# Optimization experiments

Hardware: AMD Instinct MI355X
Metric: run time of the kernel (lower is better)

The kernel has to match this reference:

```python
import jax, jax.numpy as jnp
import numpy as np

N_HEADS = 32
N_KV_HEADS = 8
HEAD_DIM = 128
GROUP = N_HEADS // N_KV_HEADS  # 4
MAX_SEQ_LEN = 4096
DIM = 3072
NEG_BIG = 1.0e9


def setup_inputs() -> dict:
    key = jax.random.key(0)
    ks = jax.random.split(key, 8)
    B, T = 1, 2048
    return {
        "x": jax.random.normal(ks[0], (B, T, DIM), dtype=jnp.float32),
        "freqs_cos": jax.random.uniform(ks[1], (T, HEAD_DIM // 2), dtype=jnp.float32),
        "freqs_sin": jax.random.uniform(ks[2], (T, HEAD_DIM // 2), dtype=jnp.float32),
        "input_pos": jnp.arange(T, dtype=jnp.int32),
        "wq": jax.random.normal(ks[3], (N_HEADS * HEAD_DIM, DIM), dtype=jnp.float32) * 0.02,
        "wk": jax.random.normal(ks[4], (N_KV_HEADS * HEAD_DIM, DIM), dtype=jnp.float32) * 0.02,
        "wv": jax.random.normal(ks[5], (N_KV_HEADS * HEAD_DIM, DIM), dtype=jnp.float32) * 0.02,
        "wo": jax.random.normal(ks[6], (DIM, N_HEADS * HEAD_DIM), dtype=jnp.float32) * 0.02,
        "k_cache": jnp.zeros((1, N_KV_HEADS, MAX_SEQ_LEN, HEAD_DIM), dtype=jnp.float32),
        "v_cache": jnp.zeros((1, N_KV_HEADS, MAX_SEQ_LEN, HEAD_DIM), dtype=jnp.float32),
    }


def _rotate_half(x):
    half = x.shape[-1] // 2
    return jnp.concatenate([-x[..., half:], x[..., :half]], axis=-1)


def _apply_rope(q, k, freqs_cos, freqs_sin):
    # freqs: [T, D/2] -> [1, T, 1, D] (tiled x2, matching torch repeat on last dim)
    fc = jnp.concatenate([freqs_cos, freqs_cos], axis=-1)[None, :, None, :]
    fs = jnp.concatenate([freqs_sin, freqs_sin], axis=-1)[None, :, None, :]
    qf = q.astype(jnp.float32)
    kf = k.astype(jnp.float32)
    q_out = qf * fc + _rotate_half(qf) * fs
    k_out = kf * fc + _rotate_half(kf) * fs
    return q_out.astype(q.dtype), k_out.astype(k.dtype)


def reference(x, freqs_cos, freqs_sin, input_pos, wq, wk, wv, wo, k_cache, v_cache):
    B, T, _ = x.shape
    # QKV projections
    q = (x @ wq.T).reshape(B, T, N_HEADS, HEAD_DIM)
    k = (x @ wk.T).reshape(B, T, N_KV_HEADS, HEAD_DIM)
    v = (x @ wv.T).reshape(B, T, N_KV_HEADS, HEAD_DIM)
    # split-half RoPE (computed in fp32)
    q, k = _apply_rope(q, k, freqs_cos, freqs_sin)
    # StaticKVCache.update: scatter [B,H,T,D] into [1,H,S,D] cache at input_pos (dim 2)
    kc = k_cache.at[:, :, input_pos].set(k.transpose(0, 2, 1, 3))
    vc = v_cache.at[:, :, input_pos].set(v.transpose(0, 2, 1, 3))
    # MetalSDPA: additive causal mask over full cache length
    S = kc.shape[2]
    k_pos = jnp.arange(S)
    valid = jnp.clip(input_pos[:, None] - k_pos[None, :] + 1, 0, 1)  # [T, S]
    mask = (valid.astype(q.dtype) - 1.0) * NEG_BIG
    # GQA attention: group q heads per kv head
    qg = q.transpose(0, 2, 1, 3).reshape(B, N_KV_HEADS, GROUP, T, HEAD_DIM)
    scale = 1.0 / jnp.sqrt(jnp.asarray(HEAD_DIM, dtype=q.dtype))
    scores = jnp.einsum('bhgtd,bhsd->bhgts', qg, kc) * scale + mask  # [B,Hk,G,T,S]
    attn = jax.nn.softmax(scores, axis=-1)
    y = jnp.einsum('bhgts,bhsd->bhgtd', attn, vc)
    y = y.reshape(B, N_HEADS, T, HEAD_DIM).transpose(0, 2, 1, 3).reshape(B, T, N_HEADS * HEAD_DIM)
    return y @ wo.T
```

## Files before the change

### kernel.cpp

```cpp
#include <hip/hip_runtime.h>

typedef __attribute__((ext_vector_type(8))) short bf16x8;
typedef __attribute__((ext_vector_type(4))) float f32x4;

#define T_SEQ   2048
#define DIM     3072
#define NQH     32
#define NKVH    8
#define HD      128
#define QDIM    4096
#define KVDIM   1024

#define AS1 __attribute__((address_space(1)))
#define AS3 __attribute__((address_space(3)))

static __device__ __forceinline__ unsigned short f2bf(float f) {
  unsigned u = __float_as_uint(f);
  u += 0x7FFFu + ((u >> 16) & 1u);
  return (unsigned short)(u >> 16);
}
static __device__ __forceinline__ float bf2f(unsigned short h) {
  return __uint_as_float(((unsigned)h) << 16);
}
static __device__ __forceinline__ unsigned pkbf(float lo, float hi) {
  unsigned r;
  asm("v_cvt_pk_bf16_f32 %0, %1, %2" : "=v"(r) : "v"(lo), "v"(hi));
  return r;
}

static __device__ __forceinline__ void gload_lds16(const unsigned short* g, unsigned short* l) {
  __builtin_amdgcn_global_load_lds((AS1 void*)(g), (AS3 void*)(l), 16, 0, 0);
}

__global__ void cvt_all(const float* __restrict__ x,  const float* __restrict__ wq,
                        const float* __restrict__ wk, const float* __restrict__ wv,
                        unsigned short* __restrict__ xb,
                        unsigned short* __restrict__ wqkvb) {
  const int N0 = 1572864;
  const int E1 = N0 + 3145728;
  const int E2 = E1 + 786432;
  const int E3 = E2 + 786432;
  const int stride = gridDim.x * blockDim.x;
  for (int i = blockIdx.x * blockDim.x + threadIdx.x; i < E3; i += stride) {
    const float* s; unsigned short* d; int off;
    if (i < N0)      { s = x;  d = xb;               off = i; }
    else if (i < E1) { s = wq; d = wqkvb;            off = i - N0; }
    else if (i < E2) { s = wk; d = wqkvb + 12582912; off = i - E1; }
    else             { s = wv; d = wqkvb + 15728640; off = i - E2; }
    float4 v = reinterpret_cast<const float4*>(s)[off];
    ushort4 o;
    o.x = f2bf(v.x); o.y = f2bf(v.y); o.z = f2bf(v.z); o.w = f2bf(v.w);
    reinterpret_cast<ushort4*>(d + (size_t)off * 4)[0] = o;
  }
}

__global__ __launch_bounds__(256) void gemm_qkv(
    const unsigned short* __restrict__ A, const unsigned short* __restrict__ B,
    const float* __restrict__ fc, const float* __restrict__ fs,
    unsigned short* __restrict__ qo, unsigned short* __restrict__ ko,
    unsigned short* __restrict__ vt,
    const float* __restrict__ wo, unsigned short* __restrict__ wob) {
  if (blockIdx.x >= 768) {
    const int total = 3145728;
    for (int i = (blockIdx.x - 768) * 256 + threadIdx.x; i < total; i += 32768) {
      float4 v = reinterpret_cast<const float4*>(wo)[i];
      ushort4 o;
      o.x = f2bf(v.x); o.y = f2bf(v.y); o.z = f2bf(v.z); o.w = f2bf(v.w);
      reinterpret_cast<ushort4*>(wob + (size_t)i * 4)[0] = o;
    }
    return;
  }
  __shared__ unsigned short epi[128 * 132];
  unsigned short* la = epi;
  unsigned short* lb = epi + 8192;
  const int K = DIM, nbx = 48;
  int bid = blockIdx.x;
  bid = (bid & 7) * 96 + (bid >> 3);
  const int bx = bid % nbx, by = bid / nbx;
  const int tid = threadIdx.x;
  const int ln = tid & 63;
  const int wave = tid >> 6;
  const int lr = ln & 15, lg = ln >> 4;
  const int rowA0 = by << 7, rowB0 = bx << 7;

  f32x4 acc[2][8] = {};

  const int ktn = K >> 6;
  for (int kt = 0; kt < ktn; kt++) {
    __syncthreads();
#pragma unroll
    for (int it = 0; it < 4; it++) {
      int ci = it * 256 + tid;
      int r = ci >> 3, cpos = ci & 7;
      int c = cpos ^ (r & 7);
      gload_lds16(A + (size_t)(rowA0 + r) * K + kt * 64 + c * 8, &la[ci * 8]);
      gload_lds16(B + (size_t)(rowB0 + r) * K + kt * 64 + c * 8, &lb[ci * 8]);
    }
    __syncthreads();
#pragma unroll
    for (int kk = 0; kk < 2; kk++) {
      bf16x8 af_[2], bf_[8];
#pragma unroll
      for (int mi = 0; mi < 2; mi++) {
        int r = wave * 32 + mi * 16 + lr;
        int p = (kk * 4 + lg) ^ (r & 7);
        af_[mi] = *reinterpret_cast<const bf16x8*>(&la[r * 64 + p * 8]);
      }
#pragma unroll
      for (int ni = 0; ni < 8; ni++) {
        int r = ni * 16 + lr;
        int p = (kk * 4 + lg) ^ (r & 7);
        bf_[ni] = *reinterpret_cast<const bf16x8*>(&lb[r * 64 + p * 8]);
      }
#pragma unroll
      for (int mi = 0; mi < 2; mi++)
#pragma unroll
        for (int ni = 0; ni < 8; ni++)
          acc[mi][ni] = __builtin_amdgcn_mfma_f32_16x16x32_bf16(af_[mi], bf_[ni], acc[mi][ni], 0, 0, 0);
    }
  }

  if (bx < 40) {
    unsigned short* dst; int dstride;
    if (bx < 32) { dst = qo + (size_t)bx * 128; dstride = QDIM; }
    else         { dst = ko + (size_t)(bx - 32) * 128; dstride = KVDIM; }
#pragma unroll
    for (int mi = 0; mi < 2; mi++)
#pragma unroll
      for (int j = 0; j < 4; j++) {
        int t = rowA0 + wave * 32 + mi * 16 + lg * 4 + j;
#pragma unroll
        for (int ni = 0; ni < 4; ni++) {
          int d = ni * 16 + lr;
          float c = fc[t * 64 + d], s = fs[t * 64 + d];
          float x0 = acc[mi][ni][j], x1 = acc[mi][ni + 4][j];
          dst[(size_t)t * dstride + d]      = f2bf(x0 * c - x1 * s);
          dst[(size_t)t * dstride + d + 64] = f2bf(x1 * c + x0 * s);
        }
      }
  } else {
    __syncthreads();
#pragma unroll
    for (int mi = 0; mi < 2; mi++)
#pragma unroll
      for (int ni = 0; ni < 8; ni++)
#pragma unroll
        for (int j = 0; j < 4; j++) {
          int r = wave * 32 + mi * 16 + lg * 4 + j;
          int cc = ni * 16 + lr;
          epi[r * 132 + cc] = f2bf(acc[mi][ni][j]);
        }
    __syncthreads();
    const int ccol = tid >> 1, th = tid & 1;
    size_t vrow = (size_t)((bx - 40) * 128 + ccol) * T_SEQ + rowA0 + th * 64;
#pragma unroll
    for (int i = 0; i < 16; i++) {
      ushort4 o;
      o.x = epi[(th * 64 + i * 4 + 0) * 132 + ccol];
      o.y = epi[(th * 64 + i * 4 + 1) * 132 + ccol];
      o.z = epi[(th * 64 + i * 4 + 2) * 132 + ccol];
      o.w = epi[(th * 64 + i * 4 + 3) * 132 + ccol];
      *reinterpret_cast<ushort4*>(&vt[vrow + i * 4]) = o;
    }
  }
}

__global__ __launch_bounds__(256) void gemm_bt(
    const unsigned short* __restrict__ A, const unsigned short* __restrict__ B,
    float* __restrict__ Cf, int M, int N, int K) {
  __shared__ unsigned short la[128 * 64];
  __shared__ unsigned short lb[128 * 64];
  const int nbx = N >> 7;
  const int q8 = gridDim.x >> 3;
  int bid = blockIdx.x;
  bid = (bid & 7) * q8 + (bid >> 3);
  const int bx = bid % nbx, by = bid / nbx;
  const int tid = threadIdx.x;
  const int ln = tid & 63;
  const int wave = tid >> 6;
  const int lr = ln & 15, lg = ln >> 4;
  const int wr = wave >> 1, wc = wave & 1;
  const int rowA0 = by << 7, rowB0 = bx << 7;

  f32x4 acc[4][4] = {};

  const int ktn = K >> 6;
  for (int kt = 0; kt < ktn; kt++) {
    __syncthreads();
#pragma unroll
    for (int it = 0; it < 4; it++) {
      int ci = it * 256 + tid;
      int r = ci >> 3, cpos = ci & 7;
      int c = cpos ^ (r & 7);
      gload_lds16(A + (size_t)(rowA0 + r) * K + kt * 64 + c * 8, &la[ci * 8]);
      gload_lds16(B + (size_t)(rowB0 + r) * K + kt * 64 + c * 8, &lb[ci * 8]);
    }
    __syncthreads();
#pragma unroll
    for (int kk = 0; kk < 2; kk++) {
      bf16x8 af[4], bfr[4];
#pragma unroll
      for (int mi = 0; mi < 4; mi++) {
        int r = wr * 64 + mi * 16 + lr;
        int p = (kk * 4 + lg) ^ (r & 7);
        af[mi] = *reinterpret_cast<const bf16x8*>(&la[r * 64 + p * 8]);
      }
#pragma unroll
      for (int ni = 0; ni < 4; ni++) {
        int r = wc * 64 + ni * 16 + lr;
        int p = (kk * 4 + lg) ^ (r & 7);
        bfr[ni] = *reinterpret_cast<const bf16x8*>(&lb[r * 64 + p * 8]);
      }
#pragma unroll
      for (int mi = 0; mi < 4; mi++)
#pragma unroll
        for (int ni = 0; ni < 4; ni++)
          acc[mi][ni] = __builtin_amdgcn_mfma_f32_16x16x32_bf16(af[mi], bfr[ni], acc[mi][ni], 0, 0, 0);
    }
  }
#pragma unroll
  for (int mi = 0; mi < 4; mi++)
#pragma unroll
    for (int ni = 0; ni < 4; ni++)
#pragma unroll
      for (int j = 0; j < 4; j++) {
        int r = rowA0 + wr * 64 + mi * 16 + lg * 4 + j;
        int cc = rowB0 + wc * 64 + ni * 16 + lr;
        Cf[(size_t)r * N + cc] = acc[mi][ni][j];
      }
}

__global__ __launch_bounds__(256) void attn_fwd(
    const unsigned short* __restrict__ q, const unsigned short* __restrict__ k,
    const unsigned short* __restrict__ vt, unsigned short* __restrict__ y) {
  __shared__ unsigned short k_lds[2][32 * 128];
  __shared__ unsigned short v_lds[2][128 * 32];
  __shared__ unsigned short p_lds[4][16 * 40];
  __shared__ float a_lds[4][16];
  const int tid = threadIdx.x;
  const int ln = tid & 63;
  const int wave = tid >> 6;
  const int lr = ln & 15, lg = ln >> 4;

  const int kh = blockIdx.x & 7;
  const int i = blockIdx.x >> 3;
  const int qh = i & 3;
  const int pr = i >> 2;
  const int qta = pr, qtb = 31 - pr;
  const int h = kh * 4 + qh;

  const int qra0 = qta * 64 + wave * 16, qrowa = qra0 + lr;
  const int qrb0 = qtb * 64 + wave * 16, qrowb = qrb0 + lr;
  const float SL2E = 0.08838834764831845f * 1.44269504088896f;
  const float NEGINF = -__builtin_inff();

  bf16x8 qfa[4], qfb[4];
  {
    const unsigned short* qba = q + (size_t)qrowa * QDIM + h * HD + lg * 8;
    const unsigned short* qbb = q + (size_t)qrowb * QDIM + h * HD + lg * 8;
#pragma unroll
    for (int dc = 0; dc < 4; dc++) {
      qfa[dc] = *reinterpret_cast<const bf16x8*>(qba + dc * 32);
      qfb[dc] = *reinterpret_cast<const bf16x8*>(qbb + dc * 32);
    }
  }

  f32x4 acca[8] = {}, accb[8] = {};
  float ma = NEGINF, la = 0.f, mb = NEGINF, lb = 0.f;

  const int krow0 = tid >> 4,  kcol0 = tid & 15;
  const int krow1 = 16 + krow0;
  const int vrow0 = tid >> 2,  vcol0 = tid & 3;
  const int vrow1 = 64 + vrow0;

  auto tile_compute = [&](int sb, int cur, const bf16x8 (&qf)[4], f32x4 (&acc)[8],
                          float& m, float& lsum, int qr0, int qrow) {
    f32x4 s0t = {0.f, 0.f, 0.f, 0.f}, s1t = {0.f, 0.f, 0.f, 0.f};
    __builtin_amdgcn_s_setprio(1);
#pragma unroll
    for (int dc = 0; dc < 4; dc++) {
      int c = lg + dc * 4;
      int p = c ^ (lr & 7);
      bf16x8 a0 = *reinterpret_cast<const bf16x8*>(&k_lds[cur][lr * 128 + p * 8]);
      bf16x8 a1 = *reinterpret_cast<const bf16x8*>(&k_lds[cur][(lr + 16) * 128 + p * 8]);
      s0t = __builtin_amdgcn_mfma_f32_16x16x32_bf16(a0, qf[dc], s0t, 0, 0, 0);
      s1t = __builtin_amdgcn_mfma_f32_16x16x32_bf16(a1, qf[dc], s1t, 0, 0, 0);
    }
    __builtin_amdgcn_s_setprio(0);

    float vv[8];
    if (sb + 31 <= qr0) {
#pragma unroll
      for (int jj = 0; jj < 4; jj++) { vv[jj] = s0t[jj]; vv[jj + 4] = s1t[jj]; }
    } else {
      const int base0 = sb + lg * 4;
#pragma unroll
      for (int jj = 0; jj < 4; jj++) {
        vv[jj]     = (base0 + jj      <= qrow) ? s0t[jj] : NEGINF;
        vv[jj + 4] = (base0 + jj + 16 <= qrow) ? s1t[jj] : NEGINF;
      }
    }

    float mx = fmaxf(fmaxf(fmaxf(vv[0], vv[1]), fmaxf(vv[2], vv[3])),
                     fmaxf(fmaxf(vv[4], vv[5]), fmaxf(vv[6], vv[7])));
    mx = fmaxf(mx, __shfl_xor(mx, 16));
    mx = fmaxf(mx, __shfl_xor(mx, 32));

    const bool doresc = __any(mx > m + 60.0f);
    const float mn = doresc ? fmaxf(m, mx) : m;

    float p[8], ps = 0.f;
#pragma unroll
    for (int ii = 0; ii < 8; ii++) { p[ii] = exp2f((vv[ii] - mn) * SL2E); ps += p[ii]; }
    ps += __shfl_xor(ps, 16);
    ps += __shfl_xor(ps, 32);

    uint2 w0, w1;
    w0.x = pkbf(p[0], p[1]); w0.y = pkbf(p[2], p[3]);
    w1.x = pkbf(p[4], p[5]); w1.y = pkbf(p[6], p[7]);
    *reinterpret_cast<uint2*>(&p_lds[wave][lr * 40 + lg * 4])      = w0;
    *reinterpret_cast<uint2*>(&p_lds[wave][lr * 40 + 16 + lg * 4]) = w1;

    if (doresc) {
      const float alpha = exp2f((m - mn) * SL2E);
      lsum = lsum * alpha + ps;
      m = mn;
      a_lds[wave][lr] = alpha;
      asm volatile("s_waitcnt lgkmcnt(0)" ::: "memory");
      float4 a4 = *reinterpret_cast<const float4*>(&a_lds[wave][lg * 4]);
#pragma unroll
      for (int dc2 = 0; dc2 < 8; dc2++) {
        acc[dc2][0] *= a4.x; acc[dc2][1] *= a4.y;
        acc[dc2][2] *= a4.z; acc[dc2][3] *= a4.w;
      }
    } else {
      lsum += ps;
      asm volatile("s_waitcnt lgkmcnt(0)" ::: "memory");
    }

    bf16x8 pa = *reinterpret_cast<const bf16x8*>(&p_lds[wave][lr * 40 + lg * 8]);
    __builtin_amdgcn_s_setprio(1);
#pragma unroll
    for (int dc2 = 0; dc2 < 8; dc2++) {
      int d = dc2 * 16 + lr;
      int p2 = lg ^ ((d >> 1) & 3);
      bf16x8 bv = *reinterpret_cast<const bf16x8*>(&v_lds[cur][d * 32 + p2 * 8]);
      acc[dc2] = __builtin_amdgcn_mfma_f32_16x16x32_bf16(pa, bv, acc[dc2], 0, 0, 0);
    }
    __builtin_amdgcn_s_setprio(0);
  };

  const int ntiles = (qtb * 64 + 95) >> 5;

  {
    bf16x8 kr0 = *reinterpret_cast<const bf16x8*>(k + (size_t)krow0 * KVDIM + kh * HD + kcol0 * 8);
    bf16x8 kr1 = *reinterpret_cast<const bf16x8*>(k + (size_t)krow1 * KVDIM + kh * HD + kcol0 * 8);
    bf16x8 vr0 = *reinterpret_cast<const bf16x8*>(vt + (size_t)(kh * HD + vrow0) * T_SEQ + vcol0 * 8);
    bf16x8 vr1 = *reinterpret_cast<const bf16x8*>(vt + (size_t)(kh * HD + vrow1) * T_SEQ + vcol0 * 8);
    *reinterpret_cast<bf16x8*>(&k_lds[0][krow0 * 128 + (kcol0 ^ (krow0 & 7)) * 8]) = kr0;
    *reinterpret_cast<bf16x8*>(&k_lds[0][krow1 * 128 + (kcol0 ^ (krow1 & 7)) * 8]) = kr1;
    *reinterpret_cast<bf16x8*>(&v_lds[0][vrow0 * 32 + (vcol0 ^ ((vrow0 >> 1) & 3)) * 8]) = vr0;
    *reinterpret_cast<bf16x8*>(&v_lds[0][vrow1 * 32 + (vcol0 ^ ((vrow1 >> 1) & 3)) * 8]) = vr1;
  }
  __syncthreads();

  for (int st = 0; st < ntiles; st++) {
    const int sb = st * 32;
    const int cur = st & 1;
    const bool more = (st + 1 < ntiles);

    bf16x8 kr0, kr1, vr0, vr1;
    if (more) {
      const int sb1 = sb + 32;
      kr0 = *reinterpret_cast<const bf16x8*>(k + (size_t)(sb1 + krow0) * KVDIM + kh * HD + kcol0 * 8);
      kr1 = *reinterpret_cast<const bf16x8*>(k + (size_t)(sb1 + krow1) * KVDIM + kh * HD + kcol0 * 8);
      vr0 = *reinterpret_cast<const bf16x8*>(vt + (size_t)(kh * HD + vrow0) * T_SEQ + sb1 + vcol0 * 8);
      vr1 = *reinterpret_cast<const bf16x8*>(vt + (size_t)(kh * HD + vrow1) * T_SEQ + sb1 + vcol0 * 8);
    }

    if (sb <= qrb0 + 15) tile_compute(sb, cur, qfb, accb, mb, lb, qrb0, qrowb);
    if (sb <= qra0 + 15) tile_compute(sb, cur, qfa, acca, ma, la, qra0, qrowa);

    if (more) {
      const int nxt = cur ^ 1;
      *reinterpret_cast<bf16x8*>(&k_lds[nxt][krow0 * 128 + (kcol0 ^ (krow0 & 7)) * 8]) = kr0;
      *reinterpret_cast<bf16x8*>(&k_lds[nxt][krow1 * 128 + (kcol0 ^ (krow1 & 7)) * 8]) = kr1;
      *reinterpret_cast<bf16x8*>(&v_lds[nxt][vrow0 * 32 + (vcol0 ^ ((vrow0 >> 1) & 3)) * 8]) = vr0;
      *reinterpret_cast<bf16x8*>(&v_lds[nxt][vrow1 * 32 + (vcol0 ^ ((vrow1 >> 1) & 3)) * 8]) = vr1;
      __syncthreads();
    }
  }

  a_lds[wave][lr] = 1.0f / lb;
  asm volatile("s_waitcnt lgkmcnt(0)" ::: "memory");
  float4 l4 = *reinterpret_cast<const float4*>(&a_lds[wave][lg * 4]);
  {
    float li[4] = {l4.x, l4.y, l4.z, l4.w};
#pragma unroll
    for (int jj = 0; jj < 4; jj++) {
      int r = qrb0 + lg * 4 + jj;
#pragma unroll
      for (int dc2 = 0; dc2 < 8; dc2++)
        y[(size_t)r * QDIM + h * HD + dc2 * 16 + lr] = f2bf(accb[dc2][jj] * li[jj]);
    }
  }
  a_lds[wave][lr] = 1.0f / la;
  asm volatile("s_waitcnt lgkmcnt(0)" ::: "memory");
  l4 = *reinterpret_cast<const float4*>(&a_lds[wave][lg * 4]);
  {
    float li[4] = {l4.x, l4.y, l4.z, l4.w};
#pragma unroll
    for (int jj = 0; jj < 4; jj++) {
      int r = qra0 + lg * 4 + jj;
#pragma unroll
      for (int dc2 = 0; dc2 < 8; dc2++)
        y[(size_t)r * QDIM + h * HD + dc2 * 16 + lr] = f2bf(acca[dc2][jj] * li[jj]);
    }
  }
}

extern "C" void kernel_launch(void* const* d_in, const int* in_sizes, int n_in,
                              void* d_out, int out_size, void* d_ws, size_t ws_size,
                              hipStream_t stream) {
  (void)in_sizes; (void)n_in; (void)out_size; (void)ws_size;
  const float* x    = (const float*)d_in[0];
  const float* fcos = (const float*)d_in[1];
  const float* fsin = (const float*)d_in[2];
  const float* wq   = (const float*)d_in[4];
  const float* wk   = (const float*)d_in[5];
  const float* wv   = (const float*)d_in[6];
  const float* wo   = (const float*)d_in[7];
  float* out = (float*)d_out;
  char* ws = (char*)d_ws;

  unsigned short* x_bf    = (unsigned short*)(ws);
  unsigned short* wqkv_bf = (unsigned short*)(ws + 12582912);
  unsigned short* q_bf    = (unsigned short*)(ws + 50331648);
  unsigned short* k_bf    = (unsigned short*)(ws + 67108864);
  unsigned short* vt_bf   = (unsigned short*)(ws + 71303168);
  unsigned short* y_bf    = (unsigned short*)(ws + 75497472);
  unsigned short* wo_bf   = (unsigned short*)(ws + 92274688);

  cvt_all<<<4096, 256, 0, stream>>>(x, wq, wk, wv, x_bf, wqkv_bf);
  gemm_qkv<<<896, 256, 0, stream>>>(x_bf, wqkv_bf, fcos, fsin, q_bf, k_bf, vt_bf, wo, wo_bf);

  attn_fwd<<<512, 256, 0, stream>>>(q_bf, k_bf, vt_bf, y_bf);

  gemm_bt<<<384, 256, 0, stream>>>(y_bf, wo_bf, out, 2048, 3072, 4096);
}
```

Baseline: 324.4 us.

## Use 2x2 wave tiling in QKV GEMM and stage RoPE epilogue through LDS

The QKV projection GEMM changes its per-wave tile from 32x128 to 64x64, arranged as a 2x2 grid of waves. Each wave now reads 8 LDS fragments per k-step instead of 10 for the same 16 MFMAs. Because a wave no longer holds both halves of a head dimension, the RoPE epilogue now writes bf16 results to LDS first, then applies rotation with coalesced packed 32-bit loads and stores. In exchange, the Q/K intermediate is rounded to bf16 before RoPE, and the epilogue pays an extra LDS round trip.

```diff
diff --git a/kernel.cpp b/kernel.cpp
--- a/kernel.cpp
+++ b/kernel.cpp
@@ -81,9 +81,10 @@
   const int ln = tid & 63;
   const int wave = tid >> 6;
   const int lr = ln & 15, lg = ln >> 4;
+  const int wr = wave >> 1, wc = wave & 1;
   const int rowA0 = by << 7, rowB0 = bx << 7;
 
-  f32x4 acc[2][8] = {};
+  f32x4 acc[4][4] = {};
 
   const int ktn = K >> 6;
   for (int kt = 0; kt < ktn; kt++) {
@@ -99,58 +100,62 @@
     __syncthreads();
 #pragma unroll
     for (int kk = 0; kk < 2; kk++) {
-      bf16x8 af_[2], bf_[8];
-#pragma unroll
-      for (int mi = 0; mi < 2; mi++) {
-        int r = wave * 32 + mi * 16 + lr;
+      bf16x8 af_[4], bf_[4];
+#pragma unroll
+      for (int mi = 0; mi < 4; mi++) {
+        int r = wr * 64 + mi * 16 + lr;
         int p = (kk * 4 + lg) ^ (r & 7);
         af_[mi] = *reinterpret_cast<const bf16x8*>(&la[r * 64 + p * 8]);
       }
 #pragma unroll
-      for (int ni = 0; ni < 8; ni++) {
-        int r = ni * 16 + lr;
+      for (int ni = 0; ni < 4; ni++) {
+        int r = wc * 64 + ni * 16 + lr;
         int p = (kk * 4 + lg) ^ (r & 7);
         bf_[ni] = *reinterpret_cast<const bf16x8*>(&lb[r * 64 + p * 8]);
       }
 #pragma unroll
-      for (int mi = 0; mi < 2; mi++)
-#pragma unroll
-        for (int ni = 0; ni < 8; ni++)
+      for (int mi = 0; mi < 4; mi++)
+#pragma unroll
+        for (int ni = 0; ni < 4; ni++)
           acc[mi][ni] = __builtin_amdgcn_mfma_f32_16x16x32_bf16(af_[mi], bf_[ni], acc[mi][ni], 0, 0, 0);
     }
   }
+
+  __syncthreads();
+#pragma unroll
+  for (int mi = 0; mi < 4; mi++)
+#pragma unroll
+    for (int ni = 0; ni < 4; ni++)
+#pragma unroll
+      for (int j = 0; j < 4; j++) {
+        int r = wr * 64 + mi * 16 + lg * 4 + j;
+        int cc = wc * 64 + ni * 16 + lr;
+        epi[r * 132 + cc] = f2bf(acc[mi][ni][j]);
+      }
+  __syncthreads();
 
   if (bx < 40) {
     unsigned short* dst; int dstride;
     if (bx < 32) { dst = qo + (size_t)bx * 128; dstride = QDIM; }
     else         { dst = ko + (size_t)(bx - 32) * 128; dstride = KVDIM; }
 #pragma unroll
-    for (int mi = 0; mi < 2; mi++)
-#pragma unroll
-      for (int j = 0; j < 4; j++) {
-        int t = rowA0 + wave * 32 + mi * 16 + lg * 4 + j;
-#pragma unroll
-        for (int ni = 0; ni < 4; ni++) {
-          int d = ni * 16 + lr;
-          float c = fc[t * 64 + d], s = fs[t * 64 + d];
-          float x0 = acc[mi][ni][j], x1 = acc[mi][ni + 4][j];
-          dst[(size_t)t * dstride + d]      = f2bf(x0 * c - x1 * s);
-          dst[(size_t)t * dstride + d + 64] = f2bf(x1 * c + x0 * s);
-        }
-      }
+    for (int w = 0; w < 16; w++) {
+      int pi = w * 256 + tid;
+      int d2 = pi & 31;
+      int r  = pi >> 5;
+      int t  = rowA0 + r;
+      unsigned lo = *reinterpret_cast<const unsigned*>(&epi[r * 132 + d2 * 2]);
+      unsigned hi = *reinterpret_cast<const unsigned*>(&epi[r * 132 + 64 + d2 * 2]);
+      float x0a = bf2f((unsigned short)(lo & 0xFFFF)), x0b = bf2f((unsigned short)(lo >> 16));
+      float x1a = bf2f((unsigned short)(hi & 0xFFFF)), x1b = bf2f((unsigned short)(hi >> 16));
+      float2 c2 = *reinterpret_cast<const float2*>(&fc[t * 64 + d2 * 2]);
+      float2 s2 = *reinterpret_cast<const float2*>(&fs[t * 64 + d2 * 2]);
+      unsigned o0 = pkbf(x0a * c2.x - x1a * s2.x, x0b * c2.y - x1b * s2.y);
+      unsigned o1 = pkbf(x1a * c2.x + x0a * s2.x, x1b * c2.y + x0b * s2.y);
+      *reinterpret_cast<unsigned*>(&dst[(size_t)t * dstride + d2 * 2])      = o0;
+      *reinterpret_cast<unsigned*>(&dst[(size_t)t * dstride + 64 + d2 * 2]) = o1;
+    }
   } else {
-    __syncthreads();
-#pragma unroll
-    for (int mi = 0; mi < 2; mi++)
-#pragma unroll
-      for (int ni = 0; ni < 8; ni++)
-#pragma unroll
-        for (int j = 0; j < 4; j++) {
-          int r = wave * 32 + mi * 16 + lg * 4 + j;
-          int cc = ni * 16 + lr;
-          epi[r * 132 + cc] = f2bf(acc[mi][ni][j]);
-        }
-    __syncthreads();
     const int ccol = tid >> 1, th = tid & 1;
     size_t vrow = (size_t)((bx - 40) * 128 + ccol) * T_SEQ + rowA0 + th * 64;
 #pragma unroll
```

Result: slower. 332.2 us (+2.4%).
